# Kernel tuning notes

Measured on AMD Instinct MI355X. Metric: run time of the kernel, lower is better.

Reference implementation:

```python
import jax, jax.numpy as jnp
import numpy as np

B, S, H = 2048, 256, 768
INNER, NB_CTX, NB_EXPERTS, NB_LABELS = 256, 2, 12, 3


def setup_inputs() -> dict:
    key = jax.random.key(0)
    ks = jax.random.split(key, 8)
    embeddings = jax.random.normal(ks[0], (B, S, H), dtype=jnp.float32)
    # spans: 1 <= stop - start <= 8, fully inside [0, S)
    starts = jax.random.randint(ks[1], (B,), 0, S - 8)
    lengths = jax.random.randint(ks[2], (B,), 1, 9)
    position_indexes = jnp.stack([starts, starts + lengths], axis=1)  # [B,2]
    categories = jax.random.randint(ks[3], (B,), 0, NB_EXPERTS)  # [B]
    # learned params (nn.Linear-style): base_linear_ : (3H -> INNER)
    W_base = jax.random.normal(ks[4], (INNER, (NB_CTX + 1) * H), dtype=jnp.float32) * 0.02
    b_base = jax.random.normal(ks[5], (INNER,), dtype=jnp.float32) * 0.02
    # 12 expert heads: (INNER -> NB_LABELS) each, stacked
    W_experts = jax.random.normal(ks[6], (NB_EXPERTS, NB_LABELS, INNER), dtype=jnp.float32) * 0.02
    b_experts = jax.random.normal(ks[7], (NB_EXPERTS, NB_LABELS), dtype=jnp.float32) * 0.02
    return {
        "embeddings": embeddings,
        "position_indexes": position_indexes,
        "categories": categories,
        "W_base": W_base,
        "b_base": b_base,
        "W_experts": W_experts,
        "b_experts": b_experts,
    }


def reference(embeddings, position_indexes, categories, W_base, b_base, W_experts, b_experts):
    b, s, h = embeddings.shape
    # same fixed numpy RNG as the torch module (seed=0): 2 random context positions
    rng = np.random.default_rng(seed=0)
    random_indexes = rng.choice(np.arange(s), size=NB_CTX)  # static, host-side
    context = embeddings[:, random_indexes, :].reshape(b, NB_CTX * h)  # [B, 2H]
    # masked mean over [start, stop) per sentence (vectorized slice+mean)
    starts = position_indexes[:, 0][:, None]
    stops = position_indexes[:, 1][:, None]
    pos = jnp.arange(s)[None, :]
    mask = ((pos >= starts) & (pos < stops)).astype(embeddings.dtype)  # [B,S]
    center = jnp.einsum("bs,bsh->bh", mask, embeddings) / mask.sum(axis=1, keepdims=True)
    feat = jnp.concatenate([center, context], axis=1)  # [B, 3H]
    hidden = jax.nn.relu(feat @ W_base.T + b_base)  # [B, INNER]
    # per-sample expert dispatch: gather expert weights, batched tiny GEMM
    W_sel = W_experts[categories]  # [B, NB_LABELS, INNER]
    b_sel = b_experts[categories]  # [B, NB_LABELS]
    out = jnp.einsum("bd,bnd->bn", hidden, W_sel) + b_sel  # [B, NB_LABELS]
    return out
```

## Files before the change

### kernel.cpp

```cpp
#include <hip/hip_runtime.h>

#define B_N 2048
#define S_N 256
#define H_N 768
#define K3 2304
#define INNER_N 256
#define IDX0 217
#define IDX1 163

typedef __attribute__((ext_vector_type(8))) short bf16x8;
typedef __attribute__((ext_vector_type(4))) float f32x4;

__device__ __forceinline__ unsigned short f2bf(float x) {
    union { float f; unsigned int u; } v;
    v.f = x;
    unsigned int u = v.u;
    unsigned int r = (u + 0x7FFFu + ((u >> 16) & 1u)) >> 16;
    return (unsigned short)r;
}

__global__ void k0_convert_w(const float* __restrict__ W, unsigned short* __restrict__ Wb) {
    int i = (blockIdx.x * 256 + threadIdx.x) * 4;
    float4 v = *(const float4*)(W + i);
    ushort4 o;
    o.x = f2bf(v.x); o.y = f2bf(v.y); o.z = f2bf(v.z); o.w = f2bf(v.w);
    *(ushort4*)(Wb + i) = o;
}

__global__ void k1_feat(const float* __restrict__ emb, const int* __restrict__ pos,
                        unsigned short* __restrict__ feat) {
    int b = blockIdx.x;
    int t = threadIdx.x;
    const float* eb = emb + (size_t)b * (S_N * H_N);
    int start = pos[2 * b], stop = pos[2 * b + 1];
    float inv = 1.0f / (float)(stop - start);
    unsigned short* fb = feat + (size_t)b * K3;
    for (int h = t; h < H_N; h += 256) {
        float s = 0.0f;
        for (int p = start; p < stop; ++p) s += eb[p * H_N + h];
        fb[h]             = f2bf(s * inv);
        fb[H_N + h]       = f2bf(eb[IDX0 * H_N + h]);
        fb[2 * H_N + h]   = f2bf(eb[IDX1 * H_N + h]);
    }
}

__global__ __launch_bounds__(256) void k2_gemm(const unsigned short* __restrict__ feat,
                                               const unsigned short* __restrict__ Wb,
                                               const float* __restrict__ bb,
                                               float* __restrict__ hidden) {
    int tid = threadIdx.x;
    int w = tid >> 6;
    int L = tid & 63;
    int lm = L & 15;
    int q = L >> 4;
    int m0 = blockIdx.x * 16;
    int n0 = blockIdx.y * 128 + w * 32;
    const short* fa = (const short*)feat + (size_t)(m0 + lm) * K3 + q * 8;
    const short* w0 = (const short*)Wb + (size_t)(n0 + lm) * K3 + q * 8;
    const short* w1 = w0 + 16 * K3;
    f32x4 acc0 = {0.f, 0.f, 0.f, 0.f};
    f32x4 acc1 = {0.f, 0.f, 0.f, 0.f};
#pragma unroll 8
    for (int k = 0; k < K3; k += 32) {
        bf16x8 a  = *(const bf16x8*)(fa + k);
        bf16x8 b0 = *(const bf16x8*)(w0 + k);
        bf16x8 b1 = *(const bf16x8*)(w1 + k);
        acc0 = __builtin_amdgcn_mfma_f32_16x16x32_bf16(a, b0, acc0, 0, 0, 0);
        acc1 = __builtin_amdgcn_mfma_f32_16x16x32_bf16(a, b1, acc1, 0, 0, 0);
    }
    int nc = n0 + lm;
    float bias0 = bb[nc];
    float bias1 = bb[nc + 16];
#pragma unroll
    for (int r = 0; r < 4; ++r) {
        int m = m0 + q * 4 + r;
        float v0 = acc0[r] + bias0;
        float v1 = acc1[r] + bias1;
        hidden[(size_t)m * INNER_N + nc]      = v0 > 0.f ? v0 : 0.f;
        hidden[(size_t)m * INNER_N + nc + 16] = v1 > 0.f ? v1 : 0.f;
    }
}

__global__ void k3_experts(const float* __restrict__ hidden, const int* __restrict__ cat,
                           const float* __restrict__ We, const float* __restrict__ be,
                           float* __restrict__ out) {
    int b = blockIdx.x * 4 + (threadIdx.x >> 6);
    int L = threadIdx.x & 63;
    float4 h = *(const float4*)(hidden + (size_t)b * INNER_N + L * 4);
    int c = cat[b];
    const float* W = We + c * (3 * INNER_N);
    float4 wv0 = *(const float4*)(W + 0 * INNER_N + L * 4);
    float4 wv1 = *(const float4*)(W + 1 * INNER_N + L * 4);
    float4 wv2 = *(const float4*)(W + 2 * INNER_N + L * 4);
    float r0 = h.x * wv0.x + h.y * wv0.y + h.z * wv0.z + h.w * wv0.w;
    float r1 = h.x * wv1.x + h.y * wv1.y + h.z * wv1.z + h.w * wv1.w;
    float r2 = h.x * wv2.x + h.y * wv2.y + h.z * wv2.z + h.w * wv2.w;
#pragma unroll
    for (int off = 32; off > 0; off >>= 1) {
        r0 += __shfl_down(r0, off);
        r1 += __shfl_down(r1, off);
        r2 += __shfl_down(r2, off);
    }
    if (L == 0) {
        out[b * 3 + 0] = r0 + be[c * 3 + 0];
        out[b * 3 + 1] = r1 + be[c * 3 + 1];
        out[b * 3 + 2] = r2 + be[c * 3 + 2];
    }
}

extern "C" void kernel_launch(void* const* d_in, const int* in_sizes, int n_in,
                              void* d_out, int out_size, void* d_ws, size_t ws_size,
                              hipStream_t stream) {
    const float* emb   = (const float*)d_in[0];
    const int*   pos   = (const int*)d_in[1];
    const int*   cat   = (const int*)d_in[2];
    const float* Wbase = (const float*)d_in[3];
    const float* bbase = (const float*)d_in[4];
    const float* Wexp  = (const float*)d_in[5];
    const float* bexp  = (const float*)d_in[6];
    float* out = (float*)d_out;

    char* ws = (char*)d_ws;
    unsigned short* Wb   = (unsigned short*)ws;
    unsigned short* feat = (unsigned short*)(ws + 1179648);
    float*          hid  = (float*)(ws + 1179648 + 9437184);

    hipLaunchKernelGGL(k0_convert_w, dim3(576), dim3(256), 0, stream, Wbase, Wb);
    hipLaunchKernelGGL(k1_feat, dim3(2048), dim3(256), 0, stream, emb, pos, feat);
    hipLaunchKernelGGL(k2_gemm, dim3(128, 2), dim3(256), 0, stream, feat, Wb, bbase, hid);
    hipLaunchKernelGGL(k3_experts, dim3(512), dim3(256), 0, stream, hid, cat, Wexp, bexp, out);
}
```

Before: 1.732 ms.

## Fuse feature gather, base GEMM and expert heads into one kernel

Replaces the separate feature-gather, base GEMM and expert-head kernels with one fused kernel. Each 512-thread block handles 8 samples: it gathers features into LDS as bf16 with float4 loads, runs the MFMA GEMM against weights repacked into an MFMA-fragment-ordered layout, keeps the hidden activations in LDS, and applies the per-sample expert head. This removes the global round trips for the feature and hidden buffers and two kernel launches, and makes the weight loads contiguous. The cost is that half of each 16-row MFMA tile is padding, the grid shrinks to 256 blocks, and every block re-reads the full packed weight matrix from cache.

```diff
diff --git a/kernel.cpp b/kernel.cpp
--- a/kernel.cpp
+++ b/kernel.cpp
@@ -7,6 +7,9 @@
 #define INNER_N 256
 #define IDX0 217
 #define IDX1 163
+#define KITERS 72
+#define ARS 2312
+#define HRS 260
 
 typedef __attribute__((ext_vector_type(8))) short bf16x8;
 typedef __attribute__((ext_vector_type(4))) float f32x4;
@@ -15,96 +18,123 @@
     union { float f; unsigned int u; } v;
     v.f = x;
     unsigned int u = v.u;
-    unsigned int r = (u + 0x7FFFu + ((u >> 16) & 1u)) >> 16;
-    return (unsigned short)r;
+    return (unsigned short)((u + 0x7FFFu + ((u >> 16) & 1u)) >> 16);
 }
 
-__global__ void k0_convert_w(const float* __restrict__ W, unsigned short* __restrict__ Wb) {
-    int i = (blockIdx.x * 256 + threadIdx.x) * 4;
-    float4 v = *(const float4*)(W + i);
-    ushort4 o;
-    o.x = f2bf(v.x); o.y = f2bf(v.y); o.z = f2bf(v.z); o.w = f2bf(v.w);
-    *(ushort4*)(Wb + i) = o;
+__global__ void k0_pack_w(const float* __restrict__ W, unsigned short* __restrict__ Wpk) {
+    int g = blockIdx.x * 256 + threadIdx.x;
+    int L = g & 63;
+    int gi = g >> 6;
+    int ki = gi % KITERS;
+    int tile = gi / KITERS;
+    int n = tile * 16 + (L & 15);
+    int k = ki * 32 + (L >> 4) * 8;
+    const float* src = W + (size_t)n * K3 + k;
+    float4 v0 = *(const float4*)(src);
+    float4 v1 = *(const float4*)(src + 4);
+    ushort4 o0, o1;
+    o0.x = f2bf(v0.x); o0.y = f2bf(v0.y); o0.z = f2bf(v0.z); o0.w = f2bf(v0.w);
+    o1.x = f2bf(v1.x); o1.y = f2bf(v1.y); o1.z = f2bf(v1.z); o1.w = f2bf(v1.w);
+    unsigned short* dst = Wpk + (size_t)g * 8;
+    *(ushort4*)(dst)     = o0;
+    *(ushort4*)(dst + 4) = o1;
 }
 
-__global__ void k1_feat(const float* __restrict__ emb, const int* __restrict__ pos,
-                        unsigned short* __restrict__ feat) {
-    int b = blockIdx.x;
-    int t = threadIdx.x;
-    const float* eb = emb + (size_t)b * (S_N * H_N);
-    int start = pos[2 * b], stop = pos[2 * b + 1];
-    float inv = 1.0f / (float)(stop - start);
-    unsigned short* fb = feat + (size_t)b * K3;
-    for (int h = t; h < H_N; h += 256) {
-        float s = 0.0f;
-        for (int p = start; p < stop; ++p) s += eb[p * H_N + h];
-        fb[h]             = f2bf(s * inv);
-        fb[H_N + h]       = f2bf(eb[IDX0 * H_N + h]);
-        fb[2 * H_N + h]   = f2bf(eb[IDX1 * H_N + h]);
-    }
-}
-
-__global__ __launch_bounds__(256) void k2_gemm(const unsigned short* __restrict__ feat,
-                                               const unsigned short* __restrict__ Wb,
-                                               const float* __restrict__ bb,
-                                               float* __restrict__ hidden) {
+__global__ __launch_bounds__(512) void k_fused(
+        const float* __restrict__ emb, const int* __restrict__ pos,
+        const int* __restrict__ cat, const unsigned short* __restrict__ Wpk,
+        const float* __restrict__ bb, const float* __restrict__ We,
+        const float* __restrict__ be, float* __restrict__ out) {
+    __shared__ unsigned short A[9 * ARS];
+    __shared__ float Hd[8 * HRS];
     int tid = threadIdx.x;
+    int b0 = blockIdx.x * 8;
     int w = tid >> 6;
     int L = tid & 63;
-    int lm = L & 15;
-    int q = L >> 4;
-    int m0 = blockIdx.x * 16;
-    int n0 = blockIdx.y * 128 + w * 32;
-    const short* fa = (const short*)feat + (size_t)(m0 + lm) * K3 + q * 8;
-    const short* w0 = (const short*)Wb + (size_t)(n0 + lm) * K3 + q * 8;
-    const short* w1 = w0 + 16 * K3;
-    f32x4 acc0 = {0.f, 0.f, 0.f, 0.f};
-    f32x4 acc1 = {0.f, 0.f, 0.f, 0.f};
-#pragma unroll 8
-    for (int k = 0; k < K3; k += 32) {
-        bf16x8 a  = *(const bf16x8*)(fa + k);
-        bf16x8 b0 = *(const bf16x8*)(w0 + k);
-        bf16x8 b1 = *(const bf16x8*)(w1 + k);
-        acc0 = __builtin_amdgcn_mfma_f32_16x16x32_bf16(a, b0, acc0, 0, 0, 0);
-        acc1 = __builtin_amdgcn_mfma_f32_16x16x32_bf16(a, b1, acc1, 0, 0, 0);
+
+    for (int i = tid; i < ARS; i += 512) A[8 * ARS + i] = 0;
+
+    {
+        int b = b0 + w;
+        const float* eb = emb + (size_t)b * (S_N * H_N);
+        int start = pos[2 * b], stop = pos[2 * b + 1];
+        float inv = 1.0f / (float)(stop - start);
+        unsigned short* arow = &A[w * ARS];
+#pragma unroll
+        for (int p = 0; p < 3; ++p) {
+            int c4 = (L + p * 64) * 4;
+            float4 s; s.x = s.y = s.z = s.w = 0.f;
+            for (int r = start; r < stop; ++r) {
+                float4 v = *(const float4*)(eb + r * H_N + c4);
+                s.x += v.x; s.y += v.y; s.z += v.z; s.w += v.w;
+            }
+            float4 c0 = *(const float4*)(eb + IDX0 * H_N + c4);
+            float4 c1 = *(const float4*)(eb + IDX1 * H_N + c4);
+            ushort4 om, o0, o1;
+            om.x = f2bf(s.x * inv); om.y = f2bf(s.y * inv);
+            om.z = f2bf(s.z * inv); om.w = f2bf(s.w * inv);
+            o0.x = f2bf(c0.x); o0.y = f2bf(c0.y); o0.z = f2bf(c0.z); o0.w = f2bf(c0.w);
+            o1.x = f2bf(c1.x); o1.y = f2bf(c1.y); o1.z = f2bf(c1.z); o1.w = f2bf(c1.w);
+            *(ushort4*)(arow + c4)            = om;
+            *(ushort4*)(arow + H_N + c4)      = o0;
+            *(ushort4*)(arow + 2 * H_N + c4)  = o1;
+        }
     }
-    int nc = n0 + lm;
-    float bias0 = bb[nc];
-    float bias1 = bb[nc + 16];
+    __syncthreads();
+
+    {
+        int lm = L & 15, q = L >> 4;
+        int arow = (lm < 8) ? lm : 8;
+        const unsigned short* a_ptr = &A[arow * ARS + q * 8];
+        const unsigned short* bp0 = Wpk + ((size_t)(2 * w) * KITERS * 64 + L) * 8;
+        const unsigned short* bp1 = Wpk + ((size_t)(2 * w + 1) * KITERS * 64 + L) * 8;
+        f32x4 acc0 = {0.f, 0.f, 0.f, 0.f};
+        f32x4 acc1 = {0.f, 0.f, 0.f, 0.f};
+#pragma unroll 4
+        for (int ki = 0; ki < KITERS; ++ki) {
+            bf16x8 a  = *(const bf16x8*)(a_ptr + ki * 32);
+            bf16x8 v0 = *(const bf16x8*)(bp0 + ki * 512);
+            bf16x8 v1 = *(const bf16x8*)(bp1 + ki * 512);
+            acc0 = __builtin_amdgcn_mfma_f32_16x16x32_bf16(a, v0, acc0, 0, 0, 0);
+            acc1 = __builtin_amdgcn_mfma_f32_16x16x32_bf16(a, v1, acc1, 0, 0, 0);
+        }
+        if (q < 2) {
+            int nc0 = w * 32 + lm, nc1 = w * 32 + 16 + lm;
+            float bias0 = bb[nc0], bias1 = bb[nc1];
 #pragma unroll
-    for (int r = 0; r < 4; ++r) {
-        int m = m0 + q * 4 + r;
-        float v0 = acc0[r] + bias0;
-        float v1 = acc1[r] + bias1;
-        hidden[(size_t)m * INNER_N + nc]      = v0 > 0.f ? v0 : 0.f;
-        hidden[(size_t)m * INNER_N + nc + 16] = v1 > 0.f ? v1 : 0.f;
+            for (int r = 0; r < 4; ++r) {
+                int m = q * 4 + r;
+                float v0 = acc0[r] + bias0;
+                float v1 = acc1[r] + bias1;
+                Hd[m * HRS + nc0] = v0 > 0.f ? v0 : 0.f;
+                Hd[m * HRS + nc1] = v1 > 0.f ? v1 : 0.f;
+            }
+        }
     }
-}
+    __syncthreads();
 
-__global__ void k3_experts(const float* __restrict__ hidden, const int* __restrict__ cat,
-                           const float* __restrict__ We, const float* __restrict__ be,
-                           float* __restrict__ out) {
-    int b = blockIdx.x * 4 + (threadIdx.x >> 6);
-    int L = threadIdx.x & 63;
-    float4 h = *(const float4*)(hidden + (size_t)b * INNER_N + L * 4);
-    int c = cat[b];
-    const float* W = We + c * (3 * INNER_N);
-    float4 wv0 = *(const float4*)(W + 0 * INNER_N + L * 4);
-    float4 wv1 = *(const float4*)(W + 1 * INNER_N + L * 4);
-    float4 wv2 = *(const float4*)(W + 2 * INNER_N + L * 4);
-    float r0 = h.x * wv0.x + h.y * wv0.y + h.z * wv0.z + h.w * wv0.w;
-    float r1 = h.x * wv1.x + h.y * wv1.y + h.z * wv1.z + h.w * wv1.w;
-    float r2 = h.x * wv2.x + h.y * wv2.y + h.z * wv2.z + h.w * wv2.w;
+    {
+        int b = b0 + w;
+        int c = cat[b];
+        float4 h = *(const float4*)(&Hd[w * HRS + 4 * L]);
+        const float* Wr = We + (size_t)c * (3 * INNER_N);
+        float4 e0 = *(const float4*)(Wr + 0 * INNER_N + 4 * L);
+        float4 e1 = *(const float4*)(Wr + 1 * INNER_N + 4 * L);
+        float4 e2 = *(const float4*)(Wr + 2 * INNER_N + 4 * L);
+        float r0 = h.x * e0.x + h.y * e0.y + h.z * e0.z + h.w * e0.w;
+        float r1 = h.x * e1.x + h.y * e1.y + h.z * e1.z + h.w * e1.w;
+        float r2 = h.x * e2.x + h.y * e2.y + h.z * e2.z + h.w * e2.w;
 #pragma unroll
-    for (int off = 32; off > 0; off >>= 1) {
-        r0 += __shfl_down(r0, off);
-        r1 += __shfl_down(r1, off);
-        r2 += __shfl_down(r2, off);
-    }
-    if (L == 0) {
-        out[b * 3 + 0] = r0 + be[c * 3 + 0];
-        out[b * 3 + 1] = r1 + be[c * 3 + 1];
-        out[b * 3 + 2] = r2 + be[c * 3 + 2];
+        for (int off = 32; off > 0; off >>= 1) {
+            r0 += __shfl_down(r0, off);
+            r1 += __shfl_down(r1, off);
+            r2 += __shfl_down(r2, off);
+        }
+        if (L == 0) {
+            out[b * 3 + 0] = r0 + be[c * 3 + 0];
+            out[b * 3 + 1] = r1 + be[c * 3 + 1];
+            out[b * 3 + 2] = r2 + be[c * 3 + 2];
+        }
     }
 }
 
@@ -120,13 +150,9 @@
     const float* bexp  = (const float*)d_in[6];
     float* out = (float*)d_out;
 
-    char* ws = (char*)d_ws;
-    unsigned short* Wb   = (unsigned short*)ws;
-    unsigned short* feat = (unsigned short*)(ws + 1179648);
-    float*          hid  = (float*)(ws + 1179648 + 9437184);
+    unsigned short* Wpk = (unsigned short*)d_ws;
 
-    hipLaunchKernelGGL(k0_convert_w, dim3(576), dim3(256), 0, stream, Wbase, Wb);
-    hipLaunchKernelGGL(k1_feat, dim3(2048), dim3(256), 0, stream, emb, pos, feat);
-    hipLaunchKernelGGL(k2_gemm, dim3(128, 2), dim3(256), 0, stream, feat, Wb, bbase, hid);
-    hipLaunchKernelGGL(k3_experts, dim3(512), dim3(256), 0, stream, hid, cat, Wexp, bexp, out);
+    hipLaunchKernelGGL(k0_pack_w, dim3(288), dim3(256), 0, stream, Wbase, Wpk);
+    hipLaunchKernelGGL(k_fused, dim3(256), dim3(512), 0, stream,
+                       emb, pos, cat, Wpk, bbase, Wexp, bexp, out);
 }
```

After: 1.708 ms. About the same (-1.4%).
